# Performance work log

Measured on AMD Instinct MI355X. Metric: run time of the kernel, lower is better.

Reference implementation:

```python
import jax, jax.numpy as jnp
import numpy as np
from jax import lax

IN_CHANNELS = 64
PYRAMID_LEVELS = 3
SIGMA = 1.6
S_VALUE = 2.0 ** (1.0 / 3.0)


def _gaussian_kernel_2d(ksize, sigma):
    # matches cv2.getGaussianKernel: normalized 1D gaussian, then outer product
    ax = np.arange(ksize, dtype=np.float64) - (ksize - 1) / 2.0
    g = np.exp(-(ax ** 2) / (2.0 * sigma ** 2))
    g = g / g.sum()
    return np.outer(g, g).astype(np.float32)


def _depthwise_kernels():
    # list of (C, 1, k, k) depthwise kernels, k = 3, 5, 7
    ks = []
    for i in range(PYRAMID_LEVELS):
        k2d = _gaussian_kernel_2d(2 * i + 3, SIGMA * (S_VALUE ** i))
        w = np.broadcast_to(k2d[None, None], (IN_CHANNELS, 1) + k2d.shape)
        ks.append(jnp.asarray(np.ascontiguousarray(w)))
    return ks


def setup_inputs() -> dict:
    key = jax.random.key(0)
    x = jax.random.normal(key, (16, IN_CHANNELS, 256, 256), dtype=jnp.float32)
    return {"x": x}


def reference(x):
    B, C, H, W = x.shape
    kernels = _depthwise_kernels()
    G = x
    pyramid = [G]
    for w in kernels:
        G = lax.conv_general_dilated(
            G, w, window_strides=(1, 1), padding="SAME",
            feature_group_count=C,
            dimension_numbers=("NCHW", "OIHW", "NCHW"))
        pyramid.append(G)
    # Laplacian levels and their sum
    L0 = pyramid[0] - pyramid[1]
    L1 = pyramid[1] - pyramid[2]
    L2 = pyramid[2] - pyramid[3]
    context = (L0 + L1 + L2).reshape(B, C, H * W)  # (B, d, HW)
    att = jnp.einsum("bdn,ben->bde", jax.nn.softmax(context, axis=2), context)
    return att
```

## Files before the change

### kernel.cpp

```cpp
#include <hip/hip_runtime.h>
#include <hip/hip_bf16.h>
#include <math.h>

typedef short bf16x8 __attribute__((ext_vector_type(8)));
typedef float f32x4  __attribute__((ext_vector_type(4)));

struct WC   { float c[13]; };
struct G157 { float g3[3], g5[5], g7[7]; };

__device__ __forceinline__ unsigned short f2bf(float f) {
  __hip_bfloat16 h = __float2bfloat16(f);
  return *reinterpret_cast<unsigned short*>(&h);
}
__device__ __forceinline__ float bf2f(unsigned short s) {
  return __uint_as_float((unsigned)s << 16);
}

__global__ __launch_bounds__(256) void zero_k(float* __restrict__ out, float* __restrict__ S,
                                              float* __restrict__ wtab, G157 gw) {
  int i = blockIdx.x * 256 + threadIdx.x;
  if (i < 65536) out[i] = 0.f;
  if (i < 1024) S[i] = 0.f;
  if (blockIdx.x == 0) {
    int g = threadIdx.x;
    float row[13];
    #pragma unroll
    for (int t = 0; t < 13; ++t) row[t] = 0.f;
    #pragma unroll
    for (int di = -3; di <= 3; ++di) {
      int ii = g + di;
      if ((unsigned)ii >= 256u) continue;
      float w7 = gw.g7[di + 3];
      #pragma unroll
      for (int dj = -2; dj <= 2; ++dj) {
        int jj = ii + dj;
        if ((unsigned)jj >= 256u) continue;
        float c2 = w7 * gw.g5[dj + 2];
        #pragma unroll
        for (int dk = -1; dk <= 1; ++dk) {
          int mm = jj + dk;
          if ((unsigned)mm >= 256u) continue;
          row[di + dj + dk + 6] += c2 * gw.g3[dk + 1];
        }
      }
    }
    #pragma unroll
    for (int t = 0; t < 13; ++t) wtab[(g << 4) + t] = row[t];
    wtab[(g << 4) + 13] = 0.f; wtab[(g << 4) + 14] = 0.f; wtab[(g << 4) + 15] = 0.f;
  }
}

__global__ __launch_bounds__(256) void ctx_k(const float* __restrict__ x,
                                             unsigned short* __restrict__ ctxb,
                                             const float* __restrict__ wtab,
                                             WC wc) {
  __shared__ __align__(16) float rb[2][4][272];
  __shared__ __align__(16) float xrb[2][4][256];
  __shared__ float vs[64][24];
  __shared__ float wl[96];

  const int tid = threadIdx.x;
  const int img = blockIdx.x >> 2;
  const int band = blockIdx.x & 3;
  const int y0 = band << 6;
  const float* xg = x + ((size_t)img << 16);
  unsigned short* cgb = ctxb + ((size_t)img << 16);

  if (tid < 96) wl[tid] = wtab[tid];
  if (tid < 128) {
    int bb = (tid >> 6) & 1, rr = (tid >> 4) & 3, pp = tid & 15;
    rb[bb][rr][(pp < 8) ? pp : (256 + pp)] = 0.f;
  }

  float win[24];
  #pragma unroll
  for (int i = 0; i < 24; ++i) win[i] = 0.f;
  #pragma unroll
  for (int i = 0; i < 20; ++i) {
    int yy = y0 - 6 + i;
    if ((unsigned)yy < 256u) win[i] = xg[yy * 256 + tid];
  }
  __syncthreads();

  const bool vsave = (tid < 12) || (tid >= 244);
  const int vsidx = (tid < 12) ? tid : (tid - 232);
  const int g = tid >> 6, q = tid & 63;

  #pragma unroll
  for (int it = 0; it < 16; ++it) {
    const int y = y0 + 4 * it;
    #pragma unroll
    for (int j = 0; j < 4; ++j) {
      if (4 * it + 14 + j < 70) {
        int yy = y + 14 + j;
        float v = 0.f;
        if (yy < 256) v = xg[yy * 256 + tid];
        win[(4 * it + 20 + j) % 24] = v;
      }
    }
    float vv[4];
    if (it > 1 && it < 14) {
      #pragma unroll
      for (int r = 0; r < 4; ++r) {
        float a = 0.f;
        #pragma unroll
        for (int t = 0; t < 13; ++t) a += wc.c[t] * win[(4 * it + r + t) % 24];
        vv[r] = a;
      }
    } else {
      #pragma unroll
      for (int r = 0; r < 4; ++r) {
        int yr = y + r;
        float a = 0.f;
        if (yr < 6) {
          #pragma unroll
          for (int t = 0; t < 13; ++t) a += wl[(yr << 4) + t] * win[(4 * it + r + t) % 24];
        } else if (yr > 249) {
          #pragma unroll
          for (int t = 0; t < 13; ++t) a += wl[((255 - yr) << 4) + (12 - t)] * win[(4 * it + r + t) % 24];
        } else {
          #pragma unroll
          for (int t = 0; t < 13; ++t) a += wc.c[t] * win[(4 * it + r + t) % 24];
        }
        vv[r] = a;
      }
    }
    const int buf = it & 1;
    #pragma unroll
    for (int r = 0; r < 4; ++r) {
      rb[buf][r][8 + tid] = vv[r];
      xrb[buf][r][tid] = win[(4 * it + 6 + r) % 24];
    }
    if (vsave) {
      #pragma unroll
      for (int r = 0; r < 4; ++r) vs[4 * it + r][vsidx] = vv[r];
    }
    __syncthreads();

    const float* hp = &rb[buf][g][4 * q];
    float f[20];
    *(float4*)&f[0]  = *(const float4*)(hp + 0);
    *(float4*)&f[4]  = *(const float4*)(hp + 4);
    *(float4*)&f[8]  = *(const float4*)(hp + 8);
    *(float4*)&f[12] = *(const float4*)(hp + 12);
    *(float4*)&f[16] = *(const float4*)(hp + 16);
    float4 xq = *(const float4*)&xrb[buf][g][4 * q];
    float h0 = 0.f, h1 = 0.f, h2 = 0.f, h3 = 0.f;
    #pragma unroll
    for (int t = 0; t < 13; ++t) {
      float w = wc.c[t];
      h0 += w * f[2 + t]; h1 += w * f[3 + t]; h2 += w * f[4 + t]; h3 += w * f[5 + t];
    }
    unsigned short s0 = f2bf(xq.x - h0), s1 = f2bf(xq.y - h1);
    unsigned short s2 = f2bf(xq.z - h2), s3 = f2bf(xq.w - h3);
    *(ushort4*)(cgb + (size_t)(y + g) * 256 + 4 * q) = make_ushort4(s0, s1, s2, s3);
  }

  __syncthreads();
  #pragma unroll
  for (int k = 0; k < 3; ++k) {
    int e = k * 256 + tid;
    int row = e / 12;
    int ce = e - row * 12;
    int col = (ce < 6) ? ce : (244 + ce);
    float h = 0.f;
    if (ce < 6) {
      #pragma unroll
      for (int t = 0; t < 13; ++t) {
        int vc = col - 6 + t;
        if (vc >= 0) h += wl[(col << 4) + t] * vs[row][vc];
      }
    } else {
      #pragma unroll
      for (int t = 0; t < 13; ++t) {
        int vc = col - 6 + t;
        if (vc < 256) h += wl[((255 - col) << 4) + (12 - t)] * vs[row][vc - 232];
      }
    }
    int yrow = y0 + row;
    float xval = xg[yrow * 256 + col];
    cgb[yrow * 256 + col] = f2bf(xval - h);
  }
}

__global__ __launch_bounds__(256) void att_k(const unsigned short* __restrict__ ctxb,
                                             float* __restrict__ S,
                                             float* __restrict__ attacc) {
  const int t = threadIdx.x;
  const int wv = t >> 6, lane = t & 63;
  const int rw = lane & 15;
  const int kq = lane >> 4;
  const int ci = blockIdx.x;
  const int b = blockIdx.y;
  const unsigned short* cb = ctxb + ((size_t)b << 22);
  const int n0 = (ci << 10) + (kq << 3);

  const unsigned short* pA = cb + (((size_t)(16 * wv + rw)) << 16) + n0;
  const unsigned short* pB = cb + (((size_t)rw) << 16) + n0;

  f32x4 acc0 = {0.f, 0.f, 0.f, 0.f}, acc1 = acc0, acc2 = acc0, acc3 = acc0;
  float ssum = 0.f;

  #pragma unroll 8
  for (int ks = 0; ks < 1024; ks += 32) {
    bf16x8 av = *(const bf16x8*)(pA + ks);
    bf16x8 ev;
    const unsigned* au = (const unsigned*)&av;
    unsigned* eu = (unsigned*)&ev;
    #pragma unroll
    for (int j = 0; j < 4; ++j) {
      unsigned w = au[j];
      float elo = __expf(__uint_as_float(w << 16));
      float ehi = __expf(__uint_as_float(w & 0xffff0000u));
      ssum += elo + ehi;
      eu[j] = ((unsigned)f2bf(ehi) << 16) | (unsigned)f2bf(elo);
    }
    bf16x8 b0 = *(const bf16x8*)(pB + ks);
    bf16x8 b1 = *(const bf16x8*)(pB + (size_t)(16 << 16) + ks);
    bf16x8 b2 = *(const bf16x8*)(pB + (size_t)(32 << 16) + ks);
    bf16x8 b3 = *(const bf16x8*)(pB + (size_t)(48 << 16) + ks);
    acc0 = __builtin_amdgcn_mfma_f32_16x16x32_bf16(ev, b0, acc0, 0, 0, 0);
    acc1 = __builtin_amdgcn_mfma_f32_16x16x32_bf16(ev, b1, acc1, 0, 0, 0);
    acc2 = __builtin_amdgcn_mfma_f32_16x16x32_bf16(ev, b2, acc2, 0, 0, 0);
    acc3 = __builtin_amdgcn_mfma_f32_16x16x32_bf16(ev, b3, acc3, 0, 0, 0);
  }

  ssum += __shfl_xor(ssum, 16);
  ssum += __shfl_xor(ssum, 32);
  if (lane < 16) atomicAdd(&S[(b << 6) + (wv << 4) + rw], ssum);

  const int dl = kq << 2;
  float* ap = attacc + (((size_t)((b << 6) + (wv << 4) + dl)) << 6) + rw;
  #pragma unroll
  for (int reg = 0; reg < 4; ++reg) {
    atomicAdd(ap + ((size_t)reg << 6) + 0,  acc0[reg]);
    atomicAdd(ap + ((size_t)reg << 6) + 16, acc1[reg]);
    atomicAdd(ap + ((size_t)reg << 6) + 32, acc2[reg]);
    atomicAdd(ap + ((size_t)reg << 6) + 48, acc3[reg]);
  }
}

__global__ __launch_bounds__(256) void fin_k(float* __restrict__ out, const float* __restrict__ S) {
  int i = blockIdx.x * 256 + threadIdx.x;
  out[i] = out[i] / S[i >> 6];
}

extern "C" void kernel_launch(void* const* d_in, const int* in_sizes, int n_in,
                              void* d_out, int out_size, void* d_ws, size_t ws_size,
                              hipStream_t stream) {
  const float* x = (const float*)d_in[0];
  float* out = (float*)d_out;
  unsigned short* ctxb = (unsigned short*)d_ws;
  float* S    = (float*)((char*)d_ws + (size_t)67108864 * 2);
  float* wtab = (float*)((char*)d_ws + (size_t)67108864 * 2 + 4096);
  if (ws_size < (size_t)67108864 * 2 + 4096 + 16384) return;

  double gg[3][7];
  double sv = pow(2.0, 1.0 / 3.0);
  for (int lv = 0; lv < 3; ++lv) {
    int k = 2 * lv + 3;
    double sig = 1.6 * pow(sv, lv), sum = 0.0;
    for (int i = 0; i < k; ++i) {
      double a = i - (k - 1) / 2.0;
      gg[lv][i] = exp(-a * a / (2.0 * sig * sig));
      sum += gg[lv][i];
    }
    for (int i = 0; i < k; ++i) gg[lv][i] /= sum;
  }

  G157 gw;
  for (int i = 0; i < 3; ++i) gw.g3[i] = (float)gg[0][i];
  for (int i = 0; i < 5; ++i) gw.g5[i] = (float)gg[1][i];
  for (int i = 0; i < 7; ++i) gw.g7[i] = (float)gg[2][i];

  WC wc;
  {
    double t35[7] = {0};
    for (int i = 0; i < 3; ++i)
      for (int j = 0; j < 5; ++j) t35[i + j] += gg[0][i] * gg[1][j];
    double t357[13] = {0};
    for (int i = 0; i < 7; ++i)
      for (int j = 0; j < 7; ++j) t357[i + j] += t35[i] * gg[2][j];
    for (int t = 0; t < 13; ++t) wc.c[t] = (float)t357[t];
  }

  zero_k<<<dim3(256), dim3(256), 0, stream>>>(out, S, wtab, gw);
  ctx_k<<<dim3(4096), dim3(256), 0, stream>>>(x, ctxb, wtab, wc);
  att_k<<<dim3(64, 16), dim3(256), 0, stream>>>(ctxb, S, out);
  fin_k<<<dim3(256), dim3(256), 0, stream>>>(out, S);
}
```

Measured before the change: 186.0 us.

## Process eight rows per iteration and reload x center from global instead of LDS

The vertical-pass loop now handles 8 rows per iteration instead of 4, which halves the number of block barriers. The sliding window grows to 32 entries so it can be indexed with a mask instead of a modulo. The LDS copy of the center x values is removed, and each thread reloads them as float4 from global memory, expecting cache hits. Boundary handling is now limited to the first and last band iterations. The cost is more registers and a second global read of x.

```diff
diff --git a/kernel.cpp b/kernel.cpp
--- a/kernel.cpp
+++ b/kernel.cpp
@@ -11,9 +11,6 @@
 __device__ __forceinline__ unsigned short f2bf(float f) {
   __hip_bfloat16 h = __float2bfloat16(f);
   return *reinterpret_cast<unsigned short*>(&h);
-}
-__device__ __forceinline__ float bf2f(unsigned short s) {
-  return __uint_as_float((unsigned)s << 16);
 }
 
 __global__ __launch_bounds__(256) void zero_k(float* __restrict__ out, float* __restrict__ S,
@@ -54,8 +51,7 @@
                                              unsigned short* __restrict__ ctxb,
                                              const float* __restrict__ wtab,
                                              WC wc) {
-  __shared__ __align__(16) float rb[2][4][272];
-  __shared__ __align__(16) float xrb[2][4][256];
+  __shared__ __align__(16) float rb[2][8][272];
   __shared__ float vs[64][24];
   __shared__ float wl[96];
 
@@ -67,14 +63,14 @@
   unsigned short* cgb = ctxb + ((size_t)img << 16);
 
   if (tid < 96) wl[tid] = wtab[tid];
-  if (tid < 128) {
-    int bb = (tid >> 6) & 1, rr = (tid >> 4) & 3, pp = tid & 15;
+  {
+    int bb = tid >> 7, rr = (tid >> 4) & 7, pp = tid & 15;
     rb[bb][rr][(pp < 8) ? pp : (256 + pp)] = 0.f;
   }
 
-  float win[24];
-  #pragma unroll
-  for (int i = 0; i < 24; ++i) win[i] = 0.f;
+  float win[32];
+  #pragma unroll
+  for (int i = 0; i < 32; ++i) win[i] = 0.f;
   #pragma unroll
   for (int i = 0; i < 20; ++i) {
     int yy = y0 - 6 + i;
@@ -87,73 +83,76 @@
   const int g = tid >> 6, q = tid & 63;
 
   #pragma unroll
-  for (int it = 0; it < 16; ++it) {
-    const int y = y0 + 4 * it;
-    #pragma unroll
-    for (int j = 0; j < 4; ++j) {
-      if (4 * it + 14 + j < 70) {
+  for (int it = 0; it < 8; ++it) {
+    const int y = y0 + 8 * it;
+    #pragma unroll
+    for (int j = 0; j < 8; ++j) {
+      if (8 * it + 14 + j < 70) {
         int yy = y + 14 + j;
         float v = 0.f;
         if (yy < 256) v = xg[yy * 256 + tid];
-        win[(4 * it + 20 + j) % 24] = v;
-      }
-    }
-    float vv[4];
-    if (it > 1 && it < 14) {
-      #pragma unroll
-      for (int r = 0; r < 4; ++r) {
+        win[(8 * it + 20 + j) & 31] = v;
+      }
+    }
+    float vv[8];
+    const bool topb = (band == 0 && it == 0), botb = (band == 3 && it == 7);
+    if (!topb && !botb) {
+      #pragma unroll
+      for (int r = 0; r < 8; ++r) {
         float a = 0.f;
         #pragma unroll
-        for (int t = 0; t < 13; ++t) a += wc.c[t] * win[(4 * it + r + t) % 24];
+        for (int t = 0; t < 13; ++t) a += wc.c[t] * win[(8 * it + r + t) & 31];
         vv[r] = a;
       }
     } else {
       #pragma unroll
-      for (int r = 0; r < 4; ++r) {
+      for (int r = 0; r < 8; ++r) {
         int yr = y + r;
         float a = 0.f;
         if (yr < 6) {
           #pragma unroll
-          for (int t = 0; t < 13; ++t) a += wl[(yr << 4) + t] * win[(4 * it + r + t) % 24];
+          for (int t = 0; t < 13; ++t) a += wl[(yr << 4) + t] * win[(8 * it + r + t) & 31];
         } else if (yr > 249) {
           #pragma unroll
-          for (int t = 0; t < 13; ++t) a += wl[((255 - yr) << 4) + (12 - t)] * win[(4 * it + r + t) % 24];
+          for (int t = 0; t < 13; ++t) a += wl[((255 - yr) << 4) + (12 - t)] * win[(8 * it + r + t) & 31];
         } else {
           #pragma unroll
-          for (int t = 0; t < 13; ++t) a += wc.c[t] * win[(4 * it + r + t) % 24];
+          for (int t = 0; t < 13; ++t) a += wc.c[t] * win[(8 * it + r + t) & 31];
         }
         vv[r] = a;
       }
     }
     const int buf = it & 1;
     #pragma unroll
-    for (int r = 0; r < 4; ++r) {
-      rb[buf][r][8 + tid] = vv[r];
-      xrb[buf][r][tid] = win[(4 * it + 6 + r) % 24];
-    }
+    for (int r = 0; r < 8; ++r) rb[buf][r][8 + tid] = vv[r];
     if (vsave) {
       #pragma unroll
-      for (int r = 0; r < 4; ++r) vs[4 * it + r][vsidx] = vv[r];
+      for (int r = 0; r < 8; ++r) vs[8 * it + r][vsidx] = vv[r];
     }
     __syncthreads();
 
-    const float* hp = &rb[buf][g][4 * q];
-    float f[20];
-    *(float4*)&f[0]  = *(const float4*)(hp + 0);
-    *(float4*)&f[4]  = *(const float4*)(hp + 4);
-    *(float4*)&f[8]  = *(const float4*)(hp + 8);
-    *(float4*)&f[12] = *(const float4*)(hp + 12);
-    *(float4*)&f[16] = *(const float4*)(hp + 16);
-    float4 xq = *(const float4*)&xrb[buf][g][4 * q];
-    float h0 = 0.f, h1 = 0.f, h2 = 0.f, h3 = 0.f;
-    #pragma unroll
-    for (int t = 0; t < 13; ++t) {
-      float w = wc.c[t];
-      h0 += w * f[2 + t]; h1 += w * f[3 + t]; h2 += w * f[4 + t]; h3 += w * f[5 + t];
-    }
-    unsigned short s0 = f2bf(xq.x - h0), s1 = f2bf(xq.y - h1);
-    unsigned short s2 = f2bf(xq.z - h2), s3 = f2bf(xq.w - h3);
-    *(ushort4*)(cgb + (size_t)(y + g) * 256 + 4 * q) = make_ushort4(s0, s1, s2, s3);
+    #pragma unroll
+    for (int u = 0; u < 2; ++u) {
+      const int rr = 2 * g + u;
+      const int yy = y + rr;
+      const float* hp = &rb[buf][rr][4 * q];
+      float f[20];
+      *(float4*)&f[0]  = *(const float4*)(hp + 0);
+      *(float4*)&f[4]  = *(const float4*)(hp + 4);
+      *(float4*)&f[8]  = *(const float4*)(hp + 8);
+      *(float4*)&f[12] = *(const float4*)(hp + 12);
+      *(float4*)&f[16] = *(const float4*)(hp + 16);
+      float4 xq = *(const float4*)(xg + yy * 256 + 4 * q);
+      float h0 = 0.f, h1 = 0.f, h2 = 0.f, h3 = 0.f;
+      #pragma unroll
+      for (int t = 0; t < 13; ++t) {
+        float w = wc.c[t];
+        h0 += w * f[2 + t]; h1 += w * f[3 + t]; h2 += w * f[4 + t]; h3 += w * f[5 + t];
+      }
+      unsigned short s0 = f2bf(xq.x - h0), s1 = f2bf(xq.y - h1);
+      unsigned short s2 = f2bf(xq.z - h2), s3 = f2bf(xq.w - h3);
+      *(ushort4*)(cgb + (size_t)yy * 256 + 4 * q) = make_ushort4(s0, s1, s2, s3);
+    }
   }
 
   __syncthreads();
```

Result: slower. 207.8 us (+11.7%).

## Split ctx_k image bands into two column halves with halo recompute

Applied to the files above, without the earlier changes.

The separable pyramid-convolution kernel now splits each 64-row band into two 128-column halves, so it runs twice as many blocks with 128 threads each. Six halo threads per block redundantly compute the vertical filter for neighbouring columns, so each block can do its horizontal pass independently. The aim is more parallelism and occupancy across CUs, traded against redundant halo loads and compute plus extra branching in the hot loop.

```diff
diff --git a/kernel.cpp b/kernel.cpp
--- a/kernel.cpp
+++ b/kernel.cpp
@@ -11,9 +11,6 @@
 __device__ __forceinline__ unsigned short f2bf(float f) {
   __hip_bfloat16 h = __float2bfloat16(f);
   return *reinterpret_cast<unsigned short*>(&h);
-}
-__device__ __forceinline__ float bf2f(unsigned short s) {
-  return __uint_as_float((unsigned)s << 16);
 }
 
 __global__ __launch_bounds__(256) void zero_k(float* __restrict__ out, float* __restrict__ S,
@@ -50,41 +47,61 @@
   }
 }
 
-__global__ __launch_bounds__(256) void ctx_k(const float* __restrict__ x,
+__global__ __launch_bounds__(128) void ctx_k(const float* __restrict__ x,
                                              unsigned short* __restrict__ ctxb,
                                              const float* __restrict__ wtab,
                                              WC wc) {
-  __shared__ __align__(16) float rb[2][4][272];
-  __shared__ __align__(16) float xrb[2][4][256];
-  __shared__ float vs[64][24];
+  __shared__ __align__(16) float rb[2][4][152];
+  __shared__ __align__(16) float xrb[2][4][128];
+  __shared__ float vs[64][12];
   __shared__ float wl[96];
 
   const int tid = threadIdx.x;
-  const int img = blockIdx.x >> 2;
-  const int band = blockIdx.x & 3;
+  const int bi = blockIdx.x;
+  const int px = bi & 1;
+  const int band = (bi >> 1) & 3;
+  const int img = bi >> 3;
   const int y0 = band << 6;
+  const int p0 = px << 7;
   const float* xg = x + ((size_t)img << 16);
   unsigned short* cgb = ctxb + ((size_t)img << 16);
 
   if (tid < 96) wl[tid] = wtab[tid];
-  if (tid < 128) {
-    int bb = (tid >> 6) & 1, rr = (tid >> 4) & 3, pp = tid & 15;
-    rb[bb][rr][(pp < 8) ? pp : (256 + pp)] = 0.f;
-  }
-
+  for (int u = tid; u < 144; u += 128) {
+    int bb = u / 72, rem = u % 72, rr = rem / 18, k = rem % 18;
+    int idx = (k < 2) ? k : ((k < 12) ? (140 + k) : (px == 0 ? (2 + k - 12) : (124 + k)));
+    rb[bb][rr][idx] = 0.f;
+  }
+
+  const int cown = p0 + tid;
   float win[24];
   #pragma unroll
   for (int i = 0; i < 24; ++i) win[i] = 0.f;
   #pragma unroll
   for (int i = 0; i < 20; ++i) {
     int yy = y0 - 6 + i;
-    if ((unsigned)yy < 256u) win[i] = xg[yy * 256 + tid];
+    if ((unsigned)yy < 256u) win[i] = xg[yy * 256 + cown];
+  }
+  const bool hal = (tid < 6);
+  const int hc = (px == 0) ? (128 + tid) : (122 + tid);
+  const int hidx = (px == 0) ? (136 + tid) : (2 + tid);
+  float win2[24];
+  #pragma unroll
+  for (int i = 0; i < 24; ++i) win2[i] = 0.f;
+  if (hal) {
+    #pragma unroll
+    for (int i = 0; i < 20; ++i) {
+      int yy = y0 - 6 + i;
+      if ((unsigned)yy < 256u) win2[i] = xg[yy * 256 + hc];
+    }
   }
   __syncthreads();
 
-  const bool vsave = (tid < 12) || (tid >= 244);
-  const int vsidx = (tid < 12) ? tid : (tid - 232);
+  const bool vsave = (px == 0) ? (tid < 12) : (tid >= 116);
+  const int vsidx = (px == 0) ? tid : (tid - 116);
   const int g = tid >> 6, q = tid & 63;
+  const int hr = (g << 1) + (q >> 5);
+  const int m = q & 31;
 
   #pragma unroll
   for (int it = 0; it < 16; ++it) {
@@ -93,12 +110,16 @@
     for (int j = 0; j < 4; ++j) {
       if (4 * it + 14 + j < 70) {
         int yy = y + 14 + j;
-        float v = 0.f;
-        if (yy < 256) v = xg[yy * 256 + tid];
+        float v = 0.f, v2 = 0.f;
+        if (yy < 256) {
+          v = xg[yy * 256 + cown];
+          if (hal) v2 = xg[yy * 256 + hc];
+        }
         win[(4 * it + 20 + j) % 24] = v;
-      }
-    }
-    float vv[4];
+        if (hal) win2[(4 * it + 20 + j) % 24] = v2;
+      }
+    }
+    float vv[4], vv2[4];
     if (it > 1 && it < 14) {
       #pragma unroll
       for (int r = 0; r < 4; ++r) {
@@ -107,22 +128,40 @@
         for (int t = 0; t < 13; ++t) a += wc.c[t] * win[(4 * it + r + t) % 24];
         vv[r] = a;
       }
+      if (hal) {
+        #pragma unroll
+        for (int r = 0; r < 4; ++r) {
+          float a = 0.f;
+          #pragma unroll
+          for (int t = 0; t < 13; ++t) a += wc.c[t] * win2[(4 * it + r + t) % 24];
+          vv2[r] = a;
+        }
+      }
     } else {
       #pragma unroll
       for (int r = 0; r < 4; ++r) {
         int yr = y + r;
-        float a = 0.f;
+        float a = 0.f, a2 = 0.f;
         if (yr < 6) {
           #pragma unroll
-          for (int t = 0; t < 13; ++t) a += wl[(yr << 4) + t] * win[(4 * it + r + t) % 24];
+          for (int t = 0; t < 13; ++t) {
+            a += wl[(yr << 4) + t] * win[(4 * it + r + t) % 24];
+            a2 += wl[(yr << 4) + t] * win2[(4 * it + r + t) % 24];
+          }
         } else if (yr > 249) {
           #pragma unroll
-          for (int t = 0; t < 13; ++t) a += wl[((255 - yr) << 4) + (12 - t)] * win[(4 * it + r + t) % 24];
+          for (int t = 0; t < 13; ++t) {
+            a += wl[((255 - yr) << 4) + (12 - t)] * win[(4 * it + r + t) % 24];
+            a2 += wl[((255 - yr) << 4) + (12 - t)] * win2[(4 * it + r + t) % 24];
+          }
         } else {
           #pragma unroll
-          for (int t = 0; t < 13; ++t) a += wc.c[t] * win[(4 * it + r + t) % 24];
+          for (int t = 0; t < 13; ++t) {
+            a += wc.c[t] * win[(4 * it + r + t) % 24];
+            a2 += wc.c[t] * win2[(4 * it + r + t) % 24];
+          }
         }
-        vv[r] = a;
+        vv[r] = a; vv2[r] = a2;
       }
     }
     const int buf = it & 1;
@@ -130,6 +169,7 @@
     for (int r = 0; r < 4; ++r) {
       rb[buf][r][8 + tid] = vv[r];
       xrb[buf][r][tid] = win[(4 * it + 6 + r) % 24];
+      if (hal) rb[buf][r][hidx] = vv2[r];
     }
     if (vsave) {
       #pragma unroll
@@ -137,14 +177,14 @@
     }
     __syncthreads();
 
-    const float* hp = &rb[buf][g][4 * q];
+    const float* hp = &rb[buf][hr][4 * m];
     float f[20];
     *(float4*)&f[0]  = *(const float4*)(hp + 0);
     *(float4*)&f[4]  = *(const float4*)(hp + 4);
     *(float4*)&f[8]  = *(const float4*)(hp + 8);
     *(float4*)&f[12] = *(const float4*)(hp + 12);
     *(float4*)&f[16] = *(const float4*)(hp + 16);
-    float4 xq = *(const float4*)&xrb[buf][g][4 * q];
+    float4 xq = *(const float4*)&xrb[buf][hr][4 * m];
     float h0 = 0.f, h1 = 0.f, h2 = 0.f, h3 = 0.f;
     #pragma unroll
     for (int t = 0; t < 13; ++t) {
@@ -153,28 +193,30 @@
     }
     unsigned short s0 = f2bf(xq.x - h0), s1 = f2bf(xq.y - h1);
     unsigned short s2 = f2bf(xq.z - h2), s3 = f2bf(xq.w - h3);
-    *(ushort4*)(cgb + (size_t)(y + g) * 256 + 4 * q) = make_ushort4(s0, s1, s2, s3);
+    *(ushort4*)(cgb + (size_t)(y + hr) * 256 + p0 + 4 * m) = make_ushort4(s0, s1, s2, s3);
   }
 
   __syncthreads();
   #pragma unroll
   for (int k = 0; k < 3; ++k) {
-    int e = k * 256 + tid;
-    int row = e / 12;
-    int ce = e - row * 12;
-    int col = (ce < 6) ? ce : (244 + ce);
+    int e = k * 128 + tid;
+    int row = e / 6;
+    int ce = e - row * 6;
     float h = 0.f;
-    if (ce < 6) {
+    int col;
+    if (px == 0) {
+      col = ce;
       #pragma unroll
       for (int t = 0; t < 13; ++t) {
         int vc = col - 6 + t;
         if (vc >= 0) h += wl[(col << 4) + t] * vs[row][vc];
       }
     } else {
+      col = 250 + ce;
       #pragma unroll
       for (int t = 0; t < 13; ++t) {
         int vc = col - 6 + t;
-        if (vc < 256) h += wl[((255 - col) << 4) + (12 - t)] * vs[row][vc - 232];
+        if (vc < 256) h += wl[((255 - col) << 4) + (12 - t)] * vs[row][vc - 244];
       }
     }
     int yrow = y0 + row;
@@ -285,7 +327,7 @@
   }
 
   zero_k<<<dim3(256), dim3(256), 0, stream>>>(out, S, wtab, gw);
-  ctx_k<<<dim3(4096), dim3(256), 0, stream>>>(x, ctxb, wtab, wc);
+  ctx_k<<<dim3(8192), dim3(128), 0, stream>>>(x, ctxb, wtab, wc);
   att_k<<<dim3(64, 16), dim3(256), 0, stream>>>(ctxb, S, out);
   fin_k<<<dim3(256), dim3(256), 0, stream>>>(out, S);
 }
```

New measurement: 250.9 us. 1.35x slower.
